# Performance work log

Measured on AMD Instinct MI355X. Metric: run time of the kernel, lower is better.

The kernel has to match this reference:

```python
import jax, jax.numpy as jnp
import numpy as np

PATCH_PERCENTAGE = 0.5
THRESHOLD = 0.3
GAUSSIAN_STD = 0.25


def _center_of_gravity(line_drawing):
    # line_drawing: [B, 1, H, W]
    B, _, H, W = line_drawing.shape
    y = jnp.linspace(0.0, 1.0, H).reshape(1, 1, H, 1)
    x = jnp.linspace(0.0, 1.0, W).reshape(1, 1, 1, W)
    total = line_drawing.sum(axis=(2, 3)) + 1e-6          # [B, 1]
    cog_y = (line_drawing * y).sum(axis=(2, 3)) / total    # [B, 1]
    cog_x = (line_drawing * x).sum(axis=(2, 3)) / total    # [B, 1]
    return jnp.concatenate([cog_y, cog_x], axis=1)         # [B, 2] (y, x)


def _gaussian_weights(side, centers):
    # centers: [B, 2]; returns [B, side*side]
    lin = jnp.linspace(0.0, 1.0, side)
    gy, gx = jnp.meshgrid(lin, lin, indexing='ij')
    coords = jnp.stack([gy.ravel(), gx.ravel()], axis=1)   # [N, 2]
    d2 = ((coords[None, :, :] - centers[:, None, :]) ** 2).sum(-1)  # [B, N]
    return jnp.exp(-d2 / (2.0 * GAUSSIAN_STD ** 2))


def _selection_indices(scores, line_drawing, k):
    B, N = scores.shape
    side = int(np.sqrt(N))
    centers = _center_of_gravity(line_drawing)
    weights = _gaussian_weights(side, centers)
    weighted = scores * weights                            # [B, N]

    above = weighted > THRESHOLD                           # [B, N]
    count = above.sum(axis=1)                              # [B]
    idx = jnp.arange(N)

    # ascending above-threshold indices first (matches torch.where order)
    sort_key = jnp.where(above, idx[None, :], N + idx[None, :])
    above_sorted = jnp.argsort(sort_key, axis=1)[:, :k]    # [B, k]

    # top-k over below-threshold scores (above ones masked to -inf)
    masked = jnp.where(above, -jnp.inf, weighted)
    _, topk_masked = jax.lax.top_k(masked, k)              # [B, k]
    _, topk_all = jax.lax.top_k(weighted, k)               # [B, k]

    pos = jnp.arange(k)[None, :]                           # [1, k]
    shift = jnp.clip(pos - count[:, None], 0, k - 1)
    remaining = jnp.take_along_axis(topk_masked, shift, axis=1)
    combined = jnp.where(pos < count[:, None], above_sorted, remaining)

    use_topk = (count >= k) | (count == 0)                 # [B]
    return jnp.where(use_topk[:, None], topk_all, combined)


def setup_inputs() -> dict:
    key = jax.random.key(0)
    k1, k2, k3, k4 = jax.random.split(key, 4)
    B, N, D, HW = 64, 784, 768, 448
    return {
        'magno_patches': jax.random.normal(k1, (B, N, D), dtype=jnp.float32),
        'vit_positional_embedding': jax.random.normal(k2, (1, N + 1, D), dtype=jnp.float32),
        'scores': jax.random.uniform(k3, (B, N), dtype=jnp.float32),
        'line_drawing': jax.random.uniform(k4, (B, 1, HW, HW), dtype=jnp.float32),
    }


def reference(magno_patches, vit_positional_embedding, scores, line_drawing):
    B, N, D = magno_patches.shape
    k = int(N * PATCH_PERCENTAGE)
    sel = _selection_indices(scores, line_drawing, k)       # [B, k] int32

    sel_patches = jnp.take_along_axis(magno_patches, sel[:, :, None], axis=1)
    pos_embed = jnp.broadcast_to(vit_positional_embedding[:, 1:, :], (B, N, D))
    sel_pos = jnp.take_along_axis(pos_embed, sel[:, :, None], axis=1)
    return sel_patches + sel_pos
```

## Files before the change

kernel.cpp:

```cpp
#include <hip/hip_runtime.h>
#include <math.h>

#define BATCH 64
#define NPATCH 784
#define DIM 768
#define KSEL 392
#define SIDE 28
#define HWDIM 448
#define NPIX (HWDIM*HWDIM)
#define PARTS 49
#define PIX_PER_PART (NPIX/PARTS)
#define GSPLIT 16
#define IPB 49

typedef float f4v __attribute__((ext_vector_type(4)));
typedef unsigned long long u64;

__global__ __launch_bounds__(256) void cog_partial(const float* __restrict__ ld,
                                                   double* __restrict__ part) {
    const int blk = blockIdx.x;
    const int b = blk / PARTS;
    const int p = blk % PARTS;
    const int t = threadIdx.x;
    const int wid = t >> 6;
    const int lane = t & 63;

    __shared__ alignas(16) float lin[HWDIM];
    for (int e = t; e < HWDIM; e += 256) lin[e] = (float)((double)e / 447.0);
    __syncthreads();

    const float* base = ld + (size_t)b * NPIX + (size_t)p * PIX_PER_PART;
    double s = 0.0, sy = 0.0, sx = 0.0;

    #pragma unroll
    for (int r = 0; r < 4; ++r) {
        const int f4 = r * 256 + t;
        const int pix = p * PIX_PER_PART + f4 * 4;
        const f4v v = reinterpret_cast<const f4v*>(base)[f4];
        const int i = pix / HWDIM;
        const int j = pix - i * HWDIM;
        const float yf = lin[i];
        const f4v xq = *reinterpret_cast<const f4v*>(&lin[j]);
        s  += (double)v.x + (double)v.y + (double)v.z + (double)v.w;
        sy += (double)__fmul_rn(v.x, yf) + (double)__fmul_rn(v.y, yf)
            + (double)__fmul_rn(v.z, yf) + (double)__fmul_rn(v.w, yf);
        sx += (double)__fmul_rn(v.x, xq.x) + (double)__fmul_rn(v.y, xq.y)
            + (double)__fmul_rn(v.z, xq.z) + (double)__fmul_rn(v.w, xq.w);
    }

    #pragma unroll
    for (int off = 32; off > 0; off >>= 1) {
        s  += __shfl_down(s, off);
        sy += __shfl_down(sy, off);
        sx += __shfl_down(sx, off);
    }

    __shared__ double red[3][4];
    if (lane == 0) { red[0][wid] = s; red[1][wid] = sy; red[2][wid] = sx; }
    __syncthreads();
    if (t == 0) {
        double* dst = part + (size_t)(b * PARTS + p) * 3;
        dst[0] = (red[0][0] + red[0][1]) + (red[0][2] + red[0][3]);
        dst[1] = (red[1][0] + red[1][1]) + (red[1][2] + red[1][3]);
        dst[2] = (red[2][0] + red[2][1]) + (red[2][2] + red[2][3]);
    }
}

__global__ __launch_bounds__(256) void select_gather(
        const float* __restrict__ scores,
        const double* __restrict__ part,
        const float* __restrict__ magno,
        const float* __restrict__ pos,
        float* __restrict__ out) {
    const int blk = blockIdx.x;
    const int b = blk / GSPLIT;
    const int g = blk % GSPLIT;
    const int t = threadIdx.x;
    const int wid = t >> 6;
    const int lane = t & 63;

    __shared__ double sd[3][64];
    __shared__ float scog[2];
    __shared__ alignas(16) u64 skey[NPATCH];
    __shared__ u64 ajm[16];
    __shared__ int sred[IPB * 4];
    __shared__ unsigned spair[IPB];
    __shared__ int snsel;

    if (t < 64) {
        if (t < PARTS) {
            const double* src = part + (size_t)(b * PARTS + t) * 3;
            sd[0][t] = src[0]; sd[1][t] = src[1]; sd[2][t] = src[2];
        } else {
            sd[0][t] = 0.0; sd[1][t] = 0.0; sd[2][t] = 0.0;
        }
    }
    __syncthreads();
    for (int off = 32; off > 0; off >>= 1) {
        if (t < off) {
            sd[0][t] += sd[0][t + off];
            sd[1][t] += sd[1][t + off];
            sd[2][t] += sd[2][t + off];
        }
        __syncthreads();
    }
    if (t == 0) {
        const float total = __fadd_rn((float)sd[0][0], 1e-6f);
        scog[0] = __fdiv_rn((float)sd[1][0], total);
        scog[1] = __fdiv_rn((float)sd[2][0], total);
    }
    __syncthreads();
    const float cy = scog[0];
    const float cx = scog[1];

    #pragma unroll
    for (int pass = 0; pass < 4; ++pass) {
        const int n = pass * 256 + t;
        const bool valid = n < NPATCH;
        float wt = 0.0f;
        if (valid) {
            const int r = n / SIDE;
            const int c = n - r * SIDE;
            const float gy = (float)((double)r / 27.0);
            const float gx = (float)((double)c / 27.0);
            const float dy = gy - cy;
            const float dx = gx - cx;
            const float dy2 = __fmul_rn(dy, dy);
            const float dx2 = __fmul_rn(dx, dx);
            const float d2 = __fadd_rn(dy2, dx2);
            const float w = (float)exp((double)(-8.0f * d2));
            wt = __fmul_rn(scores[(size_t)b * NPATCH + n], w);
            skey[n] = ((u64)__float_as_uint(wt) << 10) | (u64)(1023 - n);
        }
        const u64 m = __ballot(valid && (wt > 0.3f));
        if (lane == 0) ajm[pass * 4 + wid] = m;
    }
    __syncthreads();

    if (t < IPB * 4) {
        const int e = t >> 2;
        const int q = t & 3;
        const u64 ki = skey[g * IPB + e];
        const int j0 = q * 196;
        int r0 = 0, r1 = 0, r2 = 0, r3 = 0;
        #pragma unroll 4
        for (int j = j0; j < j0 + 196; j += 4) {
            r0 += skey[j + 0] > ki;
            r1 += skey[j + 1] > ki;
            r2 += skey[j + 2] > ki;
            r3 += skey[j + 3] > ki;
        }
        sred[t] = (r0 + r1) + (r2 + r3);
    }
    __syncthreads();

    if (t < 64) {
        int mydst = KSEL;
        int mysrc = 0;
        if (t < IPB) {
            const int i = g * IPB + t;
            const int r_all = (sred[t * 4] + sred[t * 4 + 1])
                            + (sred[t * 4 + 2] + sred[t * 4 + 3]);

            int count = 0;
            #pragma unroll
            for (int q = 0; q < 16; ++q) count += __popcll(ajm[q]);

            const int qi = i >> 6;
            const bool above_i = (ajm[qi] >> (u64)(i & 63)) & 1ull;
            int r_pre = 0;
            for (int q = 0; q < qi; ++q) r_pre += __popcll(ajm[q]);
            r_pre += __popcll(ajm[qi] & ((1ull << (u64)(i & 63)) - 1ull));

            const bool use_topk = (count == 0) || (count >= KSEL);
            mydst = (!use_topk && above_i) ? r_pre : r_all;
            mysrc = i;
        }
        const bool selme = mydst < KSEL;
        const u64 mask = __ballot(selme);
        if (selme) {
            const int posi = __popcll(mask & ((1ull << (u64)t) - 1ull));
            spair[posi] = ((unsigned)mysrc << 16) | (unsigned)mydst;
        }
        if (t == 0) snsel = (int)__popcll(mask);
    }
    __syncthreads();

    const int nsel = snsel;
    for (int e = wid; e < nsel; e += 4) {
        const unsigned pr = spair[e];
        const int srcn = (int)(pr >> 16);
        const int dslot = (int)(pr & 0xffffu);
        const f4v* src = reinterpret_cast<const f4v*>(magno + ((size_t)b * NPATCH + srcn) * DIM);
        const f4v* pp  = reinterpret_cast<const f4v*>(pos + (size_t)(srcn + 1) * DIM);
        f4v* dq = reinterpret_cast<f4v*>(out + ((size_t)b * KSEL + dslot) * DIM);
        const f4v a0 = src[lane], a1 = src[64 + lane], a2 = src[128 + lane];
        const f4v p0 = pp[lane],  p1 = pp[64 + lane],  p2 = pp[128 + lane];
        __builtin_nontemporal_store(a0 + p0, dq + lane);
        __builtin_nontemporal_store(a1 + p1, dq + 64 + lane);
        __builtin_nontemporal_store(a2 + p2, dq + 128 + lane);
    }
}

extern "C" void kernel_launch(void* const* d_in, const int* in_sizes, int n_in,
                              void* d_out, int out_size, void* d_ws, size_t ws_size,
                              hipStream_t stream) {
    const float* magno  = (const float*)d_in[0];
    const float* vit    = (const float*)d_in[1];
    const float* scores = (const float*)d_in[2];
    const float* ld     = (const float*)d_in[3];
    float* out = (float*)d_out;

    double* partials = (double*)d_ws;

    cog_partial<<<dim3(BATCH * PARTS), dim3(256), 0, stream>>>(ld, partials);
    select_gather<<<dim3(BATCH * GSPLIT), dim3(256), 0, stream>>>(scores, partials,
                                                                  magno, vit, out);
}
```

Baseline: 47.41 us.

## Split selection across more blocks and gather two rows per wave

Raises blocks per batch from 16 to 49, each ranking 16 patches. The rank count is spread over 16 threads per patch instead of 4, so all 256 threads are busy and the serial comparison loop per thread is shorter. The gather loop now handles two rows per wavefront per iteration to raise memory-level parallelism. The trade-off is that every block still recomputes the CoG reduction and all 784 weights, so that redundant work grows about threefold.

```diff
diff --git a/kernel.cpp b/kernel.cpp
--- a/kernel.cpp
+++ b/kernel.cpp
@@ -10,8 +10,8 @@
 #define NPIX (HWDIM*HWDIM)
 #define PARTS 49
 #define PIX_PER_PART (NPIX/PARTS)
-#define GSPLIT 16
-#define IPB 49
+#define GSPLIT 49
+#define IPB 16
 
 typedef float f4v __attribute__((ext_vector_type(4)));
 typedef unsigned long long u64;
@@ -83,7 +83,7 @@
     __shared__ float scog[2];
     __shared__ alignas(16) u64 skey[NPATCH];
     __shared__ u64 ajm[16];
-    __shared__ int sred[IPB * 4];
+    __shared__ int sred[IPB * 16];
     __shared__ unsigned spair[IPB];
     __shared__ int snsel;
 
@@ -137,20 +137,15 @@
     }
     __syncthreads();
 
-    if (t < IPB * 4) {
-        const int e = t >> 2;
-        const int q = t & 3;
+    {
+        const int e = t >> 4;
+        const int q = t & 15;
         const u64 ki = skey[g * IPB + e];
-        const int j0 = q * 196;
-        int r0 = 0, r1 = 0, r2 = 0, r3 = 0;
-        #pragma unroll 4
-        for (int j = j0; j < j0 + 196; j += 4) {
-            r0 += skey[j + 0] > ki;
-            r1 += skey[j + 1] > ki;
-            r2 += skey[j + 2] > ki;
-            r3 += skey[j + 3] > ki;
-        }
-        sred[t] = (r0 + r1) + (r2 + r3);
+        const int j0 = q * 49;
+        int rsum = 0;
+        #pragma unroll
+        for (int j = 0; j < 49; ++j) rsum += skey[j0 + j] > ki;
+        sred[t] = rsum;
     }
     __syncthreads();
 
@@ -159,8 +154,9 @@
         int mysrc = 0;
         if (t < IPB) {
             const int i = g * IPB + t;
-            const int r_all = (sred[t * 4] + sred[t * 4 + 1])
-                            + (sred[t * 4 + 2] + sred[t * 4 + 3]);
+            int r_all = 0;
+            #pragma unroll
+            for (int q = 0; q < 16; ++q) r_all += sred[t * 16 + q];
 
             int count = 0;
             #pragma unroll
@@ -187,18 +183,38 @@
     __syncthreads();
 
     const int nsel = snsel;
-    for (int e = wid; e < nsel; e += 4) {
-        const unsigned pr = spair[e];
-        const int srcn = (int)(pr >> 16);
-        const int dslot = (int)(pr & 0xffffu);
-        const f4v* src = reinterpret_cast<const f4v*>(magno + ((size_t)b * NPATCH + srcn) * DIM);
-        const f4v* pp  = reinterpret_cast<const f4v*>(pos + (size_t)(srcn + 1) * DIM);
-        f4v* dq = reinterpret_cast<f4v*>(out + ((size_t)b * KSEL + dslot) * DIM);
-        const f4v a0 = src[lane], a1 = src[64 + lane], a2 = src[128 + lane];
-        const f4v p0 = pp[lane],  p1 = pp[64 + lane],  p2 = pp[128 + lane];
-        __builtin_nontemporal_store(a0 + p0, dq + lane);
-        __builtin_nontemporal_store(a1 + p1, dq + 64 + lane);
-        __builtin_nontemporal_store(a2 + p2, dq + 128 + lane);
+    for (int e0 = wid * 2; e0 < nsel; e0 += 8) {
+        const int e1 = e0 + 1;
+        const unsigned pr0 = spair[e0];
+        const int s0 = (int)(pr0 >> 16);
+        const int d0 = (int)(pr0 & 0xffffu);
+        const f4v* src0 = reinterpret_cast<const f4v*>(magno + ((size_t)b * NPATCH + s0) * DIM);
+        const f4v* pp0  = reinterpret_cast<const f4v*>(pos + (size_t)(s0 + 1) * DIM);
+        f4v* dq0 = reinterpret_cast<f4v*>(out + ((size_t)b * KSEL + d0) * DIM);
+        if (e1 < nsel) {
+            const unsigned pr1 = spair[e1];
+            const int s1 = (int)(pr1 >> 16);
+            const int d1 = (int)(pr1 & 0xffffu);
+            const f4v* src1 = reinterpret_cast<const f4v*>(magno + ((size_t)b * NPATCH + s1) * DIM);
+            const f4v* pp1  = reinterpret_cast<const f4v*>(pos + (size_t)(s1 + 1) * DIM);
+            f4v* dq1 = reinterpret_cast<f4v*>(out + ((size_t)b * KSEL + d1) * DIM);
+            const f4v a0 = src0[lane], a1 = src0[64 + lane], a2 = src0[128 + lane];
+            const f4v c0 = src1[lane], c1 = src1[64 + lane], c2 = src1[128 + lane];
+            const f4v p0 = pp0[lane],  p1 = pp0[64 + lane],  p2 = pp0[128 + lane];
+            const f4v q0 = pp1[lane],  q1 = pp1[64 + lane],  q2 = pp1[128 + lane];
+            __builtin_nontemporal_store(a0 + p0, dq0 + lane);
+            __builtin_nontemporal_store(a1 + p1, dq0 + 64 + lane);
+            __builtin_nontemporal_store(a2 + p2, dq0 + 128 + lane);
+            __builtin_nontemporal_store(c0 + q0, dq1 + lane);
+            __builtin_nontemporal_store(c1 + q1, dq1 + 64 + lane);
+            __builtin_nontemporal_store(c2 + q2, dq1 + 128 + lane);
+        } else {
+            const f4v a0 = src0[lane], a1 = src0[64 + lane], a2 = src0[128 + lane];
+            const f4v p0 = pp0[lane],  p1 = pp0[64 + lane],  p2 = pp0[128 + lane];
+            __builtin_nontemporal_store(a0 + p0, dq0 + lane);
+            __builtin_nontemporal_store(a1 + p1, dq0 + 64 + lane);
+            __builtin_nontemporal_store(a2 + p2, dq0 + 128 + lane);
+        }
     }
 }
 
```

New measurement: 47.42 us. About the same (+0.0%).
